# Performance work log

Measured on AMD Instinct MI355X. Metric: run time of the kernel, lower is better.

The kernel has to match this reference:

```python
import jax, jax.numpy as jnp
import numpy as np

LOG_INV_TEMP = float(np.log(1.0 / 0.07))
B, N_IMG, N_GPS, G_DIM = 256, 49, 32, 256


def setup_inputs() -> dict:
    key = jax.random.key(0)
    k1, k2 = jax.random.split(key)
    return {
        "image_g_tokens": jax.random.normal(k1, (B, N_IMG, G_DIM), dtype=jnp.float32),
        "gps_g_tokens": jax.random.normal(k2, (B, N_GPS, G_DIM), dtype=jnp.float32),
        "logit_scale": jnp.asarray(LOG_INV_TEMP, dtype=jnp.float32),
    }


def _l2norm(x, eps=1e-12):
    # matches F.normalize(p=2, dim=-1)
    n = jnp.sqrt(jnp.sum(x * x, axis=-1, keepdims=True))
    return x / jnp.maximum(n, eps)


def _ce(logits, labels):
    # mean cross-entropy with integer labels
    logz = jax.nn.logsumexp(logits, axis=1)
    picked = jnp.take_along_axis(logits, labels[:, None], axis=1)[:, 0]
    return jnp.mean(logz - picked)


def reference(image_g_tokens, gps_g_tokens, logit_scale):
    img = _l2norm(image_g_tokens)   # (B, n, d)
    gps = _l2norm(gps_g_tokens)     # (B, m, d)
    # dist not initialized -> gather is identity, global == local
    scale = jnp.minimum(jnp.exp(logit_scale), 100.0)

    # token-level max-sim: (B, G, n, m) pairwise similarities
    sims_i2g = jnp.einsum('bnd,gmd->bgnm', img, gps)
    sims_g2i = jnp.einsum('bmd,gnd->bgmn', gps, img)
    logits_i2g = jnp.mean(jnp.max(sims_i2g, axis=3), axis=2) * scale  # (B, G)
    logits_g2i = jnp.mean(jnp.max(sims_g2i, axis=3), axis=2) * scale  # (B, G)

    labels = jnp.arange(img.shape[0])
    loss = (_ce(logits_i2g, labels) + _ce(logits_g2i, labels)) / 2.0
    return loss
```

## Files before the change

kernel.cpp:

```cpp
#include <hip/hip_runtime.h>

#define BB   256
#define NIMG 49
#define NGPS 32
#define DIM  256
#define MPAD 64

typedef __attribute__((ext_vector_type(8))) __bf16 bf16x8;
typedef __attribute__((ext_vector_type(4))) float  f32x4;
typedef __attribute__((ext_vector_type(4))) unsigned int u32x4;

__device__ inline unsigned short f2bf(float f) {
  unsigned int u = __float_as_uint(f);
  u += 0x7fff + ((u >> 16) & 1);
  return (unsigned short)(u >> 16);
}

__device__ inline float max3f(float a, float b, float c) {
  return fmaxf(fmaxf(a, b), c);
}

template<int CTRL>
__device__ inline float dppmax(float v) {
  float o = __int_as_float(__builtin_amdgcn_update_dpp(0, __float_as_int(v), CTRL, 0xF, 0xF, true));
  return fmaxf(v, o);
}
template<int CTRL>
__device__ inline float dppadd(float v) {
  float o = __int_as_float(__builtin_amdgcn_update_dpp(0, __float_as_int(v), CTRL, 0xF, 0xF, true));
  return v + o;
}
__device__ inline float max16(float v) {
  v = dppmax<0xB1>(v); v = dppmax<0x4E>(v); v = dppmax<0x141>(v); v = dppmax<0x140>(v);
  return v;
}
__device__ inline float sum16(float v) {
  v = dppadd<0xB1>(v); v = dppadd<0x4E>(v); v = dppadd<0x141>(v); v = dppadd<0x140>(v);
  return v;
}

__global__ __launch_bounds__(256) void norm_kernel(
    const float* __restrict__ img, const float* __restrict__ gps,
    unsigned short* __restrict__ imgS, unsigned short* __restrict__ gpsS)
{
  int w    = (blockIdx.x * 256 + threadIdx.x) >> 6;
  int lane = threadIdx.x & 63;

  f32x4 x = (f32x4){0.f, 0.f, 0.f, 0.f};
  bool isimg; int b = 0, n = 0, g = 0, m = 0;
  if (w < BB * MPAD) {
    isimg = true; b = w >> 6; n = w & 63;
    if (n < NIMG)
      x = *reinterpret_cast<const f32x4*>(img + ((size_t)b * NIMG + n) * DIM + lane * 4);
  } else {
    isimg = false; int t = w - BB * MPAD; g = t >> 5; m = t & 31;
    x = *reinterpret_cast<const f32x4*>(gps + (size_t)t * DIM + lane * 4);
  }

  float ss = x[0]*x[0] + x[1]*x[1] + x[2]*x[2] + x[3]*x[3];
  #pragma unroll
  for (int d = 1; d < 64; d <<= 1) ss += __shfl_xor(ss, d);
  float inv = (ss > 0.f) ? (1.0f / fmaxf(sqrtf(ss), 1e-12f)) : 0.f;

  unsigned int w01 = (unsigned)f2bf(x[0]*inv) | ((unsigned)f2bf(x[1]*inv) << 16);
  unsigned int w23 = (unsigned)f2bf(x[2]*inv) | ((unsigned)f2bf(x[3]*inv) << 16);

  int L = lane;
  unsigned int a0 = __shfl(w01, 2 * L);
  unsigned int a1 = __shfl(w23, 2 * L);
  unsigned int a2 = __shfl(w01, 2 * L + 1);
  unsigned int a3 = __shfl(w23, 2 * L + 1);
  if (L < 32) {
    u32x4 v = {a0, a1, a2, a3};
    unsigned short* dst;
    if (isimg) {
      dst = imgS + (size_t)b * 16384 + L * 512 + n * 8;
    } else {
      int mt = m >> 4, c = m & 15, kc = L >> 2, grp = L & 3;
      dst = gpsS + (size_t)g * 8192 + mt * 4096 + kc * 512 + (grp * 16 + c) * 8;
    }
    *reinterpret_cast<u32x4*>(dst) = v;
  }
}

__global__ __launch_bounds__(256, 3) void pair_kernel(
    const unsigned short* __restrict__ imgS, const unsigned short* __restrict__ gpsS,
    float* __restrict__ i2g, float* __restrict__ g2i)
{
  int tid  = threadIdx.x;
  int wv   = tid >> 6;
  int lane = tid & 63;
  int c    = lane & 15;
  int b    = blockIdx.x >> 3, gc = blockIdx.x & 7;
  int wvu  = __builtin_amdgcn_readfirstlane(wv);

  __shared__ unsigned short As[8 * 4 * 64 * 8];

  {
    const unsigned short* src = imgS + (size_t)b * 16384;
    #pragma unroll
    for (int i = 0; i < 8; ++i) {
      bf16x8 v = *reinterpret_cast<const bf16x8*>(
          src + (i * 4 + (lane >> 4)) * 512 + (wvu * 16 + (lane & 15)) * 8);
      *reinterpret_cast<bf16x8*>(
          reinterpret_cast<char*>(As) + i * 4096 + wvu * 1024 + lane * 16) = v;
    }
  }
  __syncthreads();

  const char* ab = reinterpret_cast<const char*>(As) + lane * 16;

  const unsigned short* gb = gpsS + ((size_t)(gc * 32 + wvu * 8)) * 8192;
  unsigned int lane8 = lane * 8;

  #pragma unroll 1
  for (int st = 0; st < 4; ++st) {
    f32x4 acc[2][2][4];

    {
      const unsigned short* p = gb + lane8;
      bf16x8 q00 = *reinterpret_cast<const bf16x8*>(p);
      bf16x8 q01 = *reinterpret_cast<const bf16x8*>(p + 4096);
      bf16x8 q10 = *reinterpret_cast<const bf16x8*>(p + 8192);
      bf16x8 q11 = *reinterpret_cast<const bf16x8*>(p + 12288);
      bf16x8 a0 = *reinterpret_cast<const bf16x8*>(ab);
      bf16x8 a1 = *reinterpret_cast<const bf16x8*>(ab + 1024);
      bf16x8 a2 = *reinterpret_cast<const bf16x8*>(ab + 2048);
      bf16x8 a3 = *reinterpret_cast<const bf16x8*>(ab + 3072);
      const f32x4 Z = {0.f, 0.f, 0.f, 0.f};
      acc[0][0][0] = __builtin_amdgcn_mfma_f32_16x16x32_bf16(q00, a0, Z, 0, 0, 0);
      acc[0][0][1] = __builtin_amdgcn_mfma_f32_16x16x32_bf16(q00, a1, Z, 0, 0, 0);
      acc[0][0][2] = __builtin_amdgcn_mfma_f32_16x16x32_bf16(q00, a2, Z, 0, 0, 0);
      acc[0][0][3] = __builtin_amdgcn_mfma_f32_16x16x32_bf16(q00, a3, Z, 0, 0, 0);
      acc[0][1][0] = __builtin_amdgcn_mfma_f32_16x16x32_bf16(q01, a0, Z, 0, 0, 0);
      acc[0][1][1] = __builtin_amdgcn_mfma_f32_16x16x32_bf16(q01, a1, Z, 0, 0, 0);
      acc[0][1][2] = __builtin_amdgcn_mfma_f32_16x16x32_bf16(q01, a2, Z, 0, 0, 0);
      acc[0][1][3] = __builtin_amdgcn_mfma_f32_16x16x32_bf16(q01, a3, Z, 0, 0, 0);
      acc[1][0][0] = __builtin_amdgcn_mfma_f32_16x16x32_bf16(q10, a0, Z, 0, 0, 0);
      acc[1][0][1] = __builtin_amdgcn_mfma_f32_16x16x32_bf16(q10, a1, Z, 0, 0, 0);
      acc[1][0][2] = __builtin_amdgcn_mfma_f32_16x16x32_bf16(q10, a2, Z, 0, 0, 0);
      acc[1][0][3] = __builtin_amdgcn_mfma_f32_16x16x32_bf16(q10, a3, Z, 0, 0, 0);
      acc[1][1][0] = __builtin_amdgcn_mfma_f32_16x16x32_bf16(q11, a0, Z, 0, 0, 0);
      acc[1][1][1] = __builtin_amdgcn_mfma_f32_16x16x32_bf16(q11, a1, Z, 0, 0, 0);
      acc[1][1][2] = __builtin_amdgcn_mfma_f32_16x16x32_bf16(q11, a2, Z, 0, 0, 0);
      acc[1][1][3] = __builtin_amdgcn_mfma_f32_16x16x32_bf16(q11, a3, Z, 0, 0, 0);
    }

    #pragma unroll 1
    for (int kc = 1; kc < 8; ++kc) {
      const unsigned short* p = gb + kc * 512 + lane8;
      bf16x8 q00 = *reinterpret_cast<const bf16x8*>(p);
      bf16x8 q01 = *reinterpret_cast<const bf16x8*>(p + 4096);
      bf16x8 q10 = *reinterpret_cast<const bf16x8*>(p + 8192);
      bf16x8 q11 = *reinterpret_cast<const bf16x8*>(p + 12288);
      const char* ak = ab + kc * 4096;
      bf16x8 a0 = *reinterpret_cast<const bf16x8*>(ak);
      bf16x8 a1 = *reinterpret_cast<const bf16x8*>(ak + 1024);
      bf16x8 a2 = *reinterpret_cast<const bf16x8*>(ak + 2048);
      bf16x8 a3 = *reinterpret_cast<const bf16x8*>(ak + 3072);
      acc[0][0][0] = __builtin_amdgcn_mfma_f32_16x16x32_bf16(q00, a0, acc[0][0][0], 0, 0, 0);
      acc[0][0][1] = __builtin_amdgcn_mfma_f32_16x16x32_bf16(q00, a1, acc[0][0][1], 0, 0, 0);
      acc[0][0][2] = __builtin_amdgcn_mfma_f32_16x16x32_bf16(q00, a2, acc[0][0][2], 0, 0, 0);
      acc[0][0][3] = __builtin_amdgcn_mfma_f32_16x16x32_bf16(q00, a3, acc[0][0][3], 0, 0, 0);
      acc[0][1][0] = __builtin_amdgcn_mfma_f32_16x16x32_bf16(q01, a0, acc[0][1][0], 0, 0, 0);
      acc[0][1][1] = __builtin_amdgcn_mfma_f32_16x16x32_bf16(q01, a1, acc[0][1][1], 0, 0, 0);
      acc[0][1][2] = __builtin_amdgcn_mfma_f32_16x16x32_bf16(q01, a2, acc[0][1][2], 0, 0, 0);
      acc[0][1][3] = __builtin_amdgcn_mfma_f32_16x16x32_bf16(q01, a3, acc[0][1][3], 0, 0, 0);
      acc[1][0][0] = __builtin_amdgcn_mfma_f32_16x16x32_bf16(q10, a0, acc[1][0][0], 0, 0, 0);
      acc[1][0][1] = __builtin_amdgcn_mfma_f32_16x16x32_bf16(q10, a1, acc[1][0][1], 0, 0, 0);
      acc[1][0][2] = __builtin_amdgcn_mfma_f32_16x16x32_bf16(q10, a2, acc[1][0][2], 0, 0, 0);
      acc[1][0][3] = __builtin_amdgcn_mfma_f32_16x16x32_bf16(q10, a3, acc[1][0][3], 0, 0, 0);
      acc[1][1][0] = __builtin_amdgcn_mfma_f32_16x16x32_bf16(q11, a0, acc[1][1][0], 0, 0, 0);
      acc[1][1][1] = __builtin_amdgcn_mfma_f32_16x16x32_bf16(q11, a1, acc[1][1][1], 0, 0, 0);
      acc[1][1][2] = __builtin_amdgcn_mfma_f32_16x16x32_bf16(q11, a2, acc[1][1][2], 0, 0, 0);
      acc[1][1][3] = __builtin_amdgcn_mfma_f32_16x16x32_bf16(q11, a3, acc[1][1][3], 0, 0, 0);
    }

    #pragma unroll
    for (int g = 0; g < 2; ++g) {
      float vmax[4];
      #pragma unroll
      for (int hf = 0; hf < 4; ++hf) {
        float vm = fmaxf(max3f(acc[g][0][hf][0], acc[g][0][hf][1], acc[g][0][hf][2]),
                         max3f(acc[g][0][hf][3], acc[g][1][hf][0], acc[g][1][hf][1]));
        vm = max3f(vm, acc[g][1][hf][2], acc[g][1][hf][3]);
        vm = fmaxf(vm, __shfl_xor(vm, 16));
        vm = fmaxf(vm, __shfl_xor(vm, 32));
        vmax[hf] = vm;
      }
      float s = vmax[0] + vmax[1] + vmax[2] + ((c == 0) ? vmax[3] : 0.0f);
      s = sum16(s);

      float t = 0.f;
      #pragma unroll
      for (int mt = 0; mt < 2; ++mt)
        #pragma unroll
        for (int r = 0; r < 4; ++r) {
          float h3 = (c == 0) ? acc[g][mt][3][r] : -3.0e38f;
          float hm = fmaxf(max3f(acc[g][mt][0][r], acc[g][mt][1][r], acc[g][mt][2][r]), h3);
          hm = max16(hm);
          t += hm;
        }
      t += __shfl_xor(t, 16);
      t += __shfl_xor(t, 32);

      if (lane == 0) {
        int gg = gc * 32 + wvu * 8 + st * 2 + g;
        i2g[b * 256 + gg] = s * (1.0f / NIMG);
        g2i[gg * 256 + b] = t * (1.0f / NGPS);
      }
    }
    gb += 16384;
  }
}

__global__ __launch_bounds__(256) void ce_kernel(
    const float* __restrict__ i2g, const float* __restrict__ g2i,
    const float* __restrict__ lsp, float* __restrict__ partial)
{
  int b = blockIdx.x, t = threadIdx.x, lane = t & 63, wv = t >> 6;
  float s = fminf(expf(lsp[0]), 100.0f);
  float v1 = s * i2g[b * 256 + t];
  float v2 = s * g2i[b * 256 + t];

  float m1 = v1, m2 = v2;
  #pragma unroll
  for (int d = 1; d < 64; d <<= 1) {
    m1 = fmaxf(m1, __shfl_xor(m1, d));
    m2 = fmaxf(m2, __shfl_xor(m2, d));
  }
  __shared__ float sm[2][4];
  if (lane == 0) { sm[0][wv] = m1; sm[1][wv] = m2; }
  __syncthreads();
  m1 = fmaxf(fmaxf(sm[0][0], sm[0][1]), fmaxf(sm[0][2], sm[0][3]));
  m2 = fmaxf(fmaxf(sm[1][0], sm[1][1]), fmaxf(sm[1][2], sm[1][3]));

  float e1 = expf(v1 - m1), e2 = expf(v2 - m2);
  #pragma unroll
  for (int d = 1; d < 64; d <<= 1) {
    e1 += __shfl_xor(e1, d);
    e2 += __shfl_xor(e2, d);
  }
  __shared__ float se[2][4];
  if (lane == 0) { se[0][wv] = e1; se[1][wv] = e2; }
  __syncthreads();
  if (t == 0) {
    float S1 = se[0][0] + se[0][1] + se[0][2] + se[0][3];
    float S2 = se[1][0] + se[1][1] + se[1][2] + se[1][3];
    float lse1 = m1 + logf(S1);
    float lse2 = m2 + logf(S2);
    partial[b] = (lse1 - s * i2g[b * 257]) + (lse2 - s * g2i[b * 257]);
  }
}

__global__ __launch_bounds__(256) void finish_kernel(
    const float* __restrict__ partial, float* __restrict__ out)
{
  int t = threadIdx.x, lane = t & 63, wv = t >> 6;
  float v = partial[t];
  #pragma unroll
  for (int d = 1; d < 64; d <<= 1) v += __shfl_xor(v, d);
  __shared__ float sp[4];
  if (lane == 0) sp[wv] = v;
  __syncthreads();
  if (t == 0) out[0] = (sp[0] + sp[1] + sp[2] + sp[3]) * (1.0f / 512.0f);
}

extern "C" void kernel_launch(void* const* d_in, const int* in_sizes, int n_in,
                              void* d_out, int out_size, void* d_ws, size_t ws_size,
                              hipStream_t stream)
{
  const float* img = (const float*)d_in[0];
  const float* gps = (const float*)d_in[1];
  const float* lsp = (const float*)d_in[2];
  float* out = (float*)d_out;
  char* ws = (char*)d_ws;

  unsigned short* imgS = (unsigned short*)(ws);
  unsigned short* gpsS = (unsigned short*)(ws + 8388608);
  float* i2g     = (float*)(ws + 12582912);
  float* g2i     = (float*)(ws + 12845056);
  float* partial = (float*)(ws + 13107200);

  norm_kernel<<<6144, 256, 0, stream>>>(img, gps, imgS, gpsS);
  pair_kernel<<<2048, 256, 0, stream>>>(imgS, gpsS, i2g, g2i);
  ce_kernel<<<256, 256, 0, stream>>>(i2g, g2i, lsp, partial);
  finish_kernel<<<1, 256, 0, stream>>>(partial, out);
}
```

Before: 85.13 us.

## Split off 49th image token into separate dense GEMM to avoid padded MFMA tiles

```diff
diff --git a/kernel.cpp b/kernel.cpp
--- a/kernel.cpp
+++ b/kernel.cpp
@@ -41,7 +41,8 @@
 
 __global__ __launch_bounds__(256) void norm_kernel(
     const float* __restrict__ img, const float* __restrict__ gps,
-    unsigned short* __restrict__ imgS, unsigned short* __restrict__ gpsS)
+    unsigned short* __restrict__ imgS, unsigned short* __restrict__ gpsS,
+    unsigned short* __restrict__ img48F)
 {
   int w    = (blockIdx.x * 256 + threadIdx.x) >> 6;
   int lane = threadIdx.x & 63;
@@ -72,18 +73,176 @@
   unsigned int a3 = __shfl(w23, 2 * L + 1);
   if (L < 32) {
     u32x4 v = {a0, a1, a2, a3};
-    unsigned short* dst;
     if (isimg) {
-      dst = imgS + (size_t)b * 16384 + L * 512 + n * 8;
+      *reinterpret_cast<u32x4*>(imgS + (size_t)b * 16384 + L * 512 + n * 8) = v;
+      if (n == 48 && img48F) {
+        unsigned short* d48 = img48F + ((L >> 2) * 16 + (b >> 4)) * 512
+                                     + ((L & 3) * 16 + (b & 15)) * 8;
+        *reinterpret_cast<u32x4*>(d48) = v;
+      }
     } else {
       int mt = m >> 4, c = m & 15, kc = L >> 2, grp = L & 3;
-      dst = gpsS + (size_t)g * 8192 + mt * 4096 + kc * 512 + (grp * 16 + c) * 8;
-    }
-    *reinterpret_cast<u32x4*>(dst) = v;
-  }
-}
-
-__global__ __launch_bounds__(256, 3) void pair_kernel(
+      *reinterpret_cast<u32x4*>(
+          gpsS + (size_t)g * 8192 + mt * 4096 + kc * 512 + (grp * 16 + c) * 8) = v;
+    }
+  }
+}
+
+__global__ __launch_bounds__(256) void gemm48_kernel(
+    const unsigned short* __restrict__ gpsS, const unsigned short* __restrict__ img48F,
+    float* __restrict__ S48)
+{
+  int wv = threadIdx.x >> 6, lane = threadIdx.x & 63;
+  int id = blockIdx.x * 4 + wv;
+  int t  = id >> 4, bt = id & 15;
+  const unsigned short* ga = gpsS  + (size_t)t * 4096 + lane * 8;
+  const unsigned short* bb = img48F + bt * 512 + lane * 8;
+
+  f32x4 acc = (f32x4){0.f, 0.f, 0.f, 0.f};
+  #pragma unroll
+  for (int kc = 0; kc < 8; ++kc) {
+    bf16x8 a = *reinterpret_cast<const bf16x8*>(ga + kc * 512);
+    bf16x8 q = *reinterpret_cast<const bf16x8*>(bb + kc * 8192);
+    acc = __builtin_amdgcn_mfma_f32_16x16x32_bf16(a, q, acc, 0, 0, 0);
+  }
+  int grp = lane >> 4, c = lane & 15;
+  int g = t >> 1, mbase = (t & 1) * 16 + grp * 4, b = bt * 16 + c;
+  *reinterpret_cast<f32x4*>(S48 + (size_t)g * 8192 + b * 32 + mbase) = acc;
+}
+
+__global__ __launch_bounds__(256, 4) void pair3_kernel(
+    const unsigned short* __restrict__ imgS, const unsigned short* __restrict__ gpsS,
+    const float* __restrict__ S48,
+    float* __restrict__ i2g, float* __restrict__ g2i)
+{
+  int tid  = threadIdx.x;
+  int wv   = tid >> 6;
+  int lane = tid & 63;
+  int c    = lane & 15, grp = lane >> 4;
+  int b    = blockIdx.x >> 3, gc = blockIdx.x & 7;
+  int wvu  = __builtin_amdgcn_readfirstlane(wv);
+
+  __shared__ unsigned short As[8 * 3 * 64 * 8];
+
+  {
+    const unsigned short* src = imgS + (size_t)b * 16384;
+    #pragma unroll
+    for (int i = 0; i < 6; ++i) {
+      int kc = wvu * 2 + (i / 3), hf = i % 3;
+      bf16x8 v = *reinterpret_cast<const bf16x8*>(
+          src + (kc * 4 + grp) * 512 + (hf * 16 + c) * 8);
+      *reinterpret_cast<bf16x8*>(
+          reinterpret_cast<char*>(As) + (kc * 3 + hf) * 1024 + lane * 16) = v;
+    }
+  }
+  __syncthreads();
+
+  const char* ab = reinterpret_cast<const char*>(As) + lane * 16;
+  const unsigned short* gb = gpsS + ((size_t)(gc * 32 + wvu * 8)) * 8192;
+  unsigned int lane8 = lane * 8;
+
+  #pragma unroll 1
+  for (int st = 0; st < 4; ++st) {
+    f32x4 acc[2][2][3];
+
+    {
+      const unsigned short* p = gb + lane8;
+      bf16x8 q00 = *reinterpret_cast<const bf16x8*>(p);
+      bf16x8 q01 = *reinterpret_cast<const bf16x8*>(p + 4096);
+      bf16x8 q10 = *reinterpret_cast<const bf16x8*>(p + 8192);
+      bf16x8 q11 = *reinterpret_cast<const bf16x8*>(p + 12288);
+      bf16x8 a0 = *reinterpret_cast<const bf16x8*>(ab);
+      bf16x8 a1 = *reinterpret_cast<const bf16x8*>(ab + 1024);
+      bf16x8 a2 = *reinterpret_cast<const bf16x8*>(ab + 2048);
+      const f32x4 Z = {0.f, 0.f, 0.f, 0.f};
+      acc[0][0][0] = __builtin_amdgcn_mfma_f32_16x16x32_bf16(q00, a0, Z, 0, 0, 0);
+      acc[0][0][1] = __builtin_amdgcn_mfma_f32_16x16x32_bf16(q00, a1, Z, 0, 0, 0);
+      acc[0][0][2] = __builtin_amdgcn_mfma_f32_16x16x32_bf16(q00, a2, Z, 0, 0, 0);
+      acc[0][1][0] = __builtin_amdgcn_mfma_f32_16x16x32_bf16(q01, a0, Z, 0, 0, 0);
+      acc[0][1][1] = __builtin_amdgcn_mfma_f32_16x16x32_bf16(q01, a1, Z, 0, 0, 0);
+      acc[0][1][2] = __builtin_amdgcn_mfma_f32_16x16x32_bf16(q01, a2, Z, 0, 0, 0);
+      acc[1][0][0] = __builtin_amdgcn_mfma_f32_16x16x32_bf16(q10, a0, Z, 0, 0, 0);
+      acc[1][0][1] = __builtin_amdgcn_mfma_f32_16x16x32_bf16(q10, a1, Z, 0, 0, 0);
+      acc[1][0][2] = __builtin_amdgcn_mfma_f32_16x16x32_bf16(q10, a2, Z, 0, 0, 0);
+      acc[1][1][0] = __builtin_amdgcn_mfma_f32_16x16x32_bf16(q11, a0, Z, 0, 0, 0);
+      acc[1][1][1] = __builtin_amdgcn_mfma_f32_16x16x32_bf16(q11, a1, Z, 0, 0, 0);
+      acc[1][1][2] = __builtin_amdgcn_mfma_f32_16x16x32_bf16(q11, a2, Z, 0, 0, 0);
+    }
+
+    #pragma unroll 1
+    for (int kc = 1; kc < 8; ++kc) {
+      const unsigned short* p = gb + kc * 512 + lane8;
+      bf16x8 q00 = *reinterpret_cast<const bf16x8*>(p);
+      bf16x8 q01 = *reinterpret_cast<const bf16x8*>(p + 4096);
+      bf16x8 q10 = *reinterpret_cast<const bf16x8*>(p + 8192);
+      bf16x8 q11 = *reinterpret_cast<const bf16x8*>(p + 12288);
+      const char* ak = ab + kc * 3072;
+      bf16x8 a0 = *reinterpret_cast<const bf16x8*>(ak);
+      bf16x8 a1 = *reinterpret_cast<const bf16x8*>(ak + 1024);
+      bf16x8 a2 = *reinterpret_cast<const bf16x8*>(ak + 2048);
+      acc[0][0][0] = __builtin_amdgcn_mfma_f32_16x16x32_bf16(q00, a0, acc[0][0][0], 0, 0, 0);
+      acc[0][0][1] = __builtin_amdgcn_mfma_f32_16x16x32_bf16(q00, a1, acc[0][0][1], 0, 0, 0);
+      acc[0][0][2] = __builtin_amdgcn_mfma_f32_16x16x32_bf16(q00, a2, acc[0][0][2], 0, 0, 0);
+      acc[0][1][0] = __builtin_amdgcn_mfma_f32_16x16x32_bf16(q01, a0, acc[0][1][0], 0, 0, 0);
+      acc[0][1][1] = __builtin_amdgcn_mfma_f32_16x16x32_bf16(q01, a1, acc[0][1][1], 0, 0, 0);
+      acc[0][1][2] = __builtin_amdgcn_mfma_f32_16x16x32_bf16(q01, a2, acc[0][1][2], 0, 0, 0);
+      acc[1][0][0] = __builtin_amdgcn_mfma_f32_16x16x32_bf16(q10, a0, acc[1][0][0], 0, 0, 0);
+      acc[1][0][1] = __builtin_amdgcn_mfma_f32_16x16x32_bf16(q10, a1, acc[1][0][1], 0, 0, 0);
+      acc[1][0][2] = __builtin_amdgcn_mfma_f32_16x16x32_bf16(q10, a2, acc[1][0][2], 0, 0, 0);
+      acc[1][1][0] = __builtin_amdgcn_mfma_f32_16x16x32_bf16(q11, a0, acc[1][1][0], 0, 0, 0);
+      acc[1][1][1] = __builtin_amdgcn_mfma_f32_16x16x32_bf16(q11, a1, acc[1][1][1], 0, 0, 0);
+      acc[1][1][2] = __builtin_amdgcn_mfma_f32_16x16x32_bf16(q11, a2, acc[1][1][2], 0, 0, 0);
+    }
+
+    #pragma unroll
+    for (int g = 0; g < 2; ++g) {
+      int gg = gc * 32 + wvu * 8 + st * 2 + g;
+      const float* sp = S48 + (size_t)gg * 8192 + b * 32 + grp * 4;
+      f32x4 sa = *reinterpret_cast<const f32x4*>(sp);
+      f32x4 sb = *reinterpret_cast<const f32x4*>(sp + 16);
+
+      float vmax[3];
+      #pragma unroll
+      for (int hf = 0; hf < 3; ++hf) {
+        float vm = fmaxf(max3f(acc[g][0][hf][0], acc[g][0][hf][1], acc[g][0][hf][2]),
+                         max3f(acc[g][0][hf][3], acc[g][1][hf][0], acc[g][1][hf][1]));
+        vm = max3f(vm, acc[g][1][hf][2], acc[g][1][hf][3]);
+        vm = fmaxf(vm, __shfl_xor(vm, 16));
+        vm = fmaxf(vm, __shfl_xor(vm, 32));
+        vmax[hf] = vm;
+      }
+      float s = vmax[0] + vmax[1] + vmax[2];
+      s = sum16(s);
+      float m48 = fmaxf(max3f(sa[0], sa[1], sa[2]),
+                        max3f(sa[3], sb[0], sb[1]));
+      m48 = max3f(m48, sb[2], sb[3]);
+      m48 = fmaxf(m48, __shfl_xor(m48, 16));
+      m48 = fmaxf(m48, __shfl_xor(m48, 32));
+      s += m48;
+
+      float t = 0.f;
+      #pragma unroll
+      for (int mt = 0; mt < 2; ++mt)
+        #pragma unroll
+        for (int r = 0; r < 4; ++r) {
+          float s48v = (mt == 0) ? sa[r] : sb[r];
+          float hm = fmaxf(max3f(acc[g][mt][0][r], acc[g][mt][1][r], acc[g][mt][2][r]), s48v);
+          hm = max16(hm);
+          t += hm;
+        }
+      t += __shfl_xor(t, 16);
+      t += __shfl_xor(t, 32);
+
+      if (lane == 0) {
+        i2g[b * 256 + gg] = s * (1.0f / NIMG);
+        g2i[gg * 256 + b] = t * (1.0f / NGPS);
+      }
+    }
+    gb += 16384;
+  }
+}
+
+__global__ __launch_bounds__(256, 3) void pair4_kernel(
     const unsigned short* __restrict__ imgS, const unsigned short* __restrict__ gpsS,
     float* __restrict__ i2g, float* __restrict__ g2i)
 {
@@ -109,14 +268,12 @@
   __syncthreads();
 
   const char* ab = reinterpret_cast<const char*>(As) + lane * 16;
-
   const unsigned short* gb = gpsS + ((size_t)(gc * 32 + wvu * 8)) * 8192;
   unsigned int lane8 = lane * 8;
 
   #pragma unroll 1
   for (int st = 0; st < 4; ++st) {
     f32x4 acc[2][2][4];
-
     {
       const unsigned short* p = gb + lane8;
       bf16x8 q00 = *reinterpret_cast<const bf16x8*>(p);
@@ -145,7 +302,6 @@
       acc[1][1][2] = __builtin_amdgcn_mfma_f32_16x16x32_bf16(q11, a2, Z, 0, 0, 0);
       acc[1][1][3] = __builtin_amdgcn_mfma_f32_16x16x32_bf16(q11, a3, Z, 0, 0, 0);
     }
-
     #pragma unroll 1
     for (int kc = 1; kc < 8; ++kc) {
       const unsigned short* p = gb + kc * 512 + lane8;
@@ -175,7 +331,6 @@
       acc[1][1][2] = __builtin_amdgcn_mfma_f32_16x16x32_bf16(q11, a2, acc[1][1][2], 0, 0, 0);
       acc[1][1][3] = __builtin_amdgcn_mfma_f32_16x16x32_bf16(q11, a3, acc[1][1][3], 0, 0, 0);
     }
-
     #pragma unroll
     for (int g = 0; g < 2; ++g) {
       float vmax[4];
@@ -190,7 +345,6 @@
       }
       float s = vmax[0] + vmax[1] + vmax[2] + ((c == 0) ? vmax[3] : 0.0f);
       s = sum16(s);
-
       float t = 0.f;
       #pragma unroll
       for (int mt = 0; mt < 2; ++mt)
@@ -203,7 +357,6 @@
         }
       t += __shfl_xor(t, 16);
       t += __shfl_xor(t, 32);
-
       if (lane == 0) {
         int gg = gc * 32 + wvu * 8 + st * 2 + g;
         i2g[b * 256 + gg] = s * (1.0f / NIMG);
@@ -276,14 +429,28 @@
   float* out = (float*)d_out;
   char* ws = (char*)d_ws;
 
+  const size_t NEED = 21627904;
   unsigned short* imgS = (unsigned short*)(ws);
   unsigned short* gpsS = (unsigned short*)(ws + 8388608);
-  float* i2g     = (float*)(ws + 12582912);
-  float* g2i     = (float*)(ws + 12845056);
-  float* partial = (float*)(ws + 13107200);
-
-  norm_kernel<<<6144, 256, 0, stream>>>(img, gps, imgS, gpsS);
-  pair_kernel<<<2048, 256, 0, stream>>>(imgS, gpsS, i2g, g2i);
-  ce_kernel<<<256, 256, 0, stream>>>(i2g, g2i, lsp, partial);
-  finish_kernel<<<1, 256, 0, stream>>>(partial, out);
-}
+
+  if (ws_size >= NEED) {
+    unsigned short* img48F = (unsigned short*)(ws + 12582912);
+    float* S48     = (float*)(ws + 12713984);
+    float* i2g     = (float*)(ws + 21102592);
+    float* g2i     = (float*)(ws + 21364736);
+    float* partial = (float*)(ws + 21626880);
+    norm_kernel<<<6144, 256, 0, stream>>>(img, gps, imgS, gpsS, img48F);
+    gemm48_kernel<<<2048, 256, 0, stream>>>(gpsS, img48F, S48);
+    pair3_kernel<<<2048, 256, 0, stream>>>(imgS, gpsS, S48, i2g, g2i);
+    ce_kernel<<<256, 256, 0, stream>>>(i2g, g2i, lsp, partial);
+    finish_kernel<<<1, 256, 0, stream>>>(partial, out);
+  } else {
+    float* i2g     = (float*)(ws + 12582912);
+    float* g2i     = (float*)(ws + 12845056);
+    float* partial = (float*)(ws + 13107200);
+    norm_kernel<<<6144, 256, 0, stream>>>(img, gps, imgS, gpsS, nullptr);
+    pair4_kernel<<<2048, 256, 0, stream>>>(imgS, gpsS, i2g, g2i);
+    ce_kernel<<<256, 256, 0, stream>>>(i2g, g2i, lsp, partial);
+    finish_kernel<<<1, 256, 0, stream>>>(partial, out);
+  }
+}
```

Result: slower. 89.79 us (+5.5%).
